# Performance work log

Measured on AMD Instinct MI355X. Metric: run time of the kernel, lower is better.

Reference implementation:

```python
import jax, jax.numpy as jnp
import numpy as np

C = 5          # max within-cluster spike gap (module-level constant in source repo)
DELTA = 0.05   # margin constant (module-level constant in source repo)
B, T, N = 128, 512, 256


def setup_inputs() -> dict:
    key = jax.random.key(0)
    k1, k2, k3 = jax.random.split(key, 3)
    vmem = jax.random.normal(k1, (B, T, N), dtype=jnp.float32) - 1.5
    vlastmem = jax.random.normal(k2, (B, T, N), dtype=jnp.float32)  # unused by the loss math
    labels_t = jax.random.randint(k3, (B, N), 0, 4)
    ratio = jnp.float32(0.5)
    return {"vmem": vmem, "vlastmem": vlastmem, "labels_t": labels_t, "ratio": ratio}


def _per_neuron(v, key):
    """v: [T] membrane trace for one (batch, neuron). Returns (num_cluster, under_term, max_over)."""
    Tn = v.shape[0]
    t = jnp.arange(Tn)
    spike = v >= 0.0
    s = spike.astype(jnp.int32)
    # prefix sums: cs[i] = number of spikes in v[:i]
    cs = jnp.concatenate([jnp.zeros(1, jnp.int32), jnp.cumsum(s)])
    # new cluster starts at t iff spike[t] and no spike in [t-C, t-1]  (gap > C)
    prev_cnt = cs[t] - cs[jnp.clip(t - C, 0, Tn)]
    is_start = spike & (prev_cnt == 0)
    nclu = jnp.sum(is_start.astype(jnp.int32))
    # under-branch mask = union over clusters of [first-C, last+C] = C-dilation of spike train
    dil_cnt = cs[jnp.clip(t + C + 1, 0, Tn)] - cs[jnp.clip(t - C, 0, Tn)]
    mask = dil_cnt > 0

    # per-cluster stats via segmented reductions (cluster id = running count of starts)
    cid = jnp.clip(jnp.cumsum(is_start.astype(jnp.int32)) - 1, 0, Tn - 1)
    counts = jax.ops.segment_sum(s, cid, num_segments=Tn)
    first = jax.ops.segment_min(jnp.where(spike, t, Tn), cid, num_segments=Tn)
    last = jax.ops.segment_max(jnp.where(spike, t, -1), cid, num_segments=Tn)

    # over branch: cluster minimizing (end_idx - beg_idx) == min spike count (first on ties)
    counts_q = jnp.where(t < nclu, counts, Tn + 2)
    ic = jnp.argmin(counts_q)
    over_mask = (t >= first[ic]) & (t <= last[ic])
    max_over = jnp.max(jnp.where(over_mask, v, -jnp.inf))

    # under branch: if unmasked timesteps remain, penalize -max(v[mask==0]);
    # else take v at a (pinned-seed) random spike position
    has_zero = jnp.any(~mask)
    max_unmask = jnp.max(jnp.where(~mask, v, -jnp.inf))
    nsp = cs[-1]
    sorted_pos = jnp.sort(jnp.where(spike, t, Tn))
    r = jax.random.randint(key, (), 0, jnp.maximum(nsp, 1))
    v_rand = v[jnp.clip(sorted_pos[r], 0, Tn - 1)]
    under_term = jnp.where(has_zero, -max_unmask, v_rand)
    return nclu, under_term, max_over


def _forward(vmem, vlastmem, labels_t, ratio):
    Bv, Tv, Nv = vmem.shape
    vflat = jnp.swapaxes(vmem, 1, 2).reshape(Bv * Nv, Tv)   # [B*N, T]
    lflat = labels_t.reshape(Bv * Nv)
    keys = jax.random.split(jax.random.key(42), Bv * Nv)     # pinned seed for the random-spike pick
    nclu, under_term, max_over = jax.vmap(_per_neuron)(vflat, keys)
    ncf = nclu.astype(vmem.dtype)
    margin = DELTA * ratio * ncf
    under = jnp.where(lflat > nclu, under_term + margin, 0.0)
    over = jnp.where(lflat < nclu, max_over + margin, 0.0)
    loss = jnp.sum(under + over)
    spike_output = ncf.reshape(Bv, Nv)
    return loss, spike_output


def reference(vmem, vlastmem, labels_t, ratio):
    return _forward(vmem, vlastmem, labels_t, ratio)
```

## Files before the change

### kernel.cpp

```cpp
#include <hip/hip_runtime.h>
#include <stdint.h>

#define TDIM 512
#define NDIM 256
#define CGAP 5
#define DELTA_C 0.05f
#define NSEG 8
#define SEGT 64
#define BIGI (1 << 28)

typedef unsigned long long u64;
typedef unsigned int u32;


__device__ __forceinline__ int  ctz64(u64 x)   { return x ? __builtin_ctzll(x) : 64; }
__device__ __forceinline__ int  hib64(u64 x)   { return x ? 63 - __builtin_clzll(x) : -1; }
__device__ __forceinline__ u64  below64(int p) { return (p >= 64) ? ~0ull : ((1ull << p) - 1ull); }

extern "C" __global__ void __launch_bounds__(512, 2)
stca_kernel(const float* __restrict__ vmem, const int* __restrict__ labels,
            const float* __restrict__ ratio_p, float* __restrict__ out,
            float* __restrict__ ws) {
  __shared__ u32 sw_lo[NSEG * 64], sw_hi[NSEG * 64];
  __shared__ int s_nclu[NSEG * 64], s_fs[NSEG * 64], s_ls[NSEG * 64];
  __shared__ int s_pc[NSEG * 64], s_pl[NSEG * 64];
  __shared__ int s_sc[NSEG * 64], s_sf[NSEG * 64];
  __shared__ int s_bc[NSEG * 64], s_bf[NSEG * 64], s_bl[NSEG * 64];
  __shared__ int pn_nclu[64], pn_tf[64], pn_tl[64];
  __shared__ float sO[NSEG * 64], sU[NSEG * 64];

  const int lane = threadIdx.x & 63;
  const int seg  = threadIdx.x >> 6;
  const int idx  = threadIdx.x;
  const int blk  = blockIdx.x;
  const int b    = blk >> 2;
  const int n0   = (blk & 3) << 6;
  const int n    = n0 + lane;

  const float* g = vmem + (size_t)b * TDIM * NDIM + n;
  const int t0 = seg * SEGT;

  u64 s = 0ull;
#pragma unroll 1
  for (int c = 0; c < SEGT / 8; ++c) {
    const float* gp = g + (size_t)(t0 + c * 8) * NDIM;
    const float y0 = gp[0 * NDIM], y1 = gp[1 * NDIM], y2 = gp[2 * NDIM],
                y3 = gp[3 * NDIM], y4 = gp[4 * NDIM], y5 = gp[5 * NDIM],
                y6 = gp[6 * NDIM], y7 = gp[7 * NDIM];
    const u32 bits = (y0 >= 0.f ?   1u : 0u) | (y1 >= 0.f ?   2u : 0u)
                   | (y2 >= 0.f ?   4u : 0u) | (y3 >= 0.f ?   8u : 0u)
                   | (y4 >= 0.f ?  16u : 0u) | (y5 >= 0.f ?  32u : 0u)
                   | (y6 >= 0.f ?  64u : 0u) | (y7 >= 0.f ? 128u : 0u);
    s |= (u64)bits << (c * 8);
  }

  u64 w5 = (s << 1) | (s << 2);
  w5 |= (s << 3) | (s << 4) | (s << 5);
  const u64 starts = s & ~w5;
  const int nclu = __popcll(starts);
  const int fs_l = ctz64(s);
  const int ls_l = hib64(s);
  const u64 st2 = starts & (starts - 1);
  const int p2  = ctz64(st2);
  const u64 pm  = s & below64(p2);
  const int pcnt  = __popcll(pm);
  const int pls_l = hib64(pm);
  const int plast = (nclu >= 1) ? hib64(starts) : 0;
  const int scnt  = __popcll(s >> plast);
  int bcnt = BIGI, bfs_l = 0, bls_l = 0;
  u64 rem = st2;
  while ((rem & (rem - 1)) != 0ull) {
    const int p   = ctz64(rem);
    const u64 rem2 = rem & (rem - 1);
    const int pnx = ctz64(rem2);
    const u64 m   = s & below64(pnx) & ~below64(p);
    const int cnt = __popcll(m);
    if (cnt < bcnt) { bcnt = cnt; bfs_l = p; bls_l = hib64(m); }
    rem = rem2;
  }

  sw_lo[idx] = (u32)s;  sw_hi[idx] = (u32)(s >> 32);
  s_nclu[idx] = nclu;
  s_fs[idx] = (nclu >= 1) ? (t0 + fs_l) : BIGI;
  s_ls[idx] = t0 + ls_l;
  s_pc[idx] = pcnt;  s_pl[idx] = t0 + pls_l;
  s_sc[idx] = scnt;  s_sf[idx] = t0 + plast;
  s_bc[idx] = bcnt;  s_bf[idx] = t0 + bfs_l;  s_bl[idx] = t0 + bls_l;
  __syncthreads();

  const u64 sL = (seg > 0)
      ? ((u64)sw_lo[idx - 64] | ((u64)sw_hi[idx - 64] << 32)) : 0ull;
  const u64 sR = (seg < NSEG - 1)
      ? ((u64)sw_lo[idx + 64] | ((u64)sw_hi[idx + 64] << 32)) : 0ull;
  u64 D = s;
  D |= (s << 1) | (sL >> 63);
  D |= (s << 2) | (sL >> 62);
  D |= (s << 3) | (sL >> 61);
  D |= (s << 4) | (sL >> 60);
  D |= (s << 5) | (sL >> 59);
  D |= (s >> 1) | (sR << 63);
  D |= (s >> 2) | (sR << 62);
  D |= (s >> 3) | (sR << 61);
  D |= (s >> 4) | (sR << 60);
  D |= (s >> 5) | (sR << 59);

  int a_nclu = 0;
  if (seg == 0) {
    int a_fs = BIGI, a_ls = 0;
    int a_pcnt = 0, a_pls = 0, a_scnt = 0, a_sfs = 0;
    int a_bcnt = BIGI, a_bfs = 0, a_bls = 0;
    for (int sg = 0; sg < NSEG; ++sg) {
      const int j = (sg << 6) + lane;
      const int r_nclu = s_nclu[j];
      if (r_nclu == 0) continue;
      const int r_fs = s_fs[j], r_ls = s_ls[j];
      const int r_pcnt = s_pc[j], r_pls = s_pl[j];
      const int r_scnt = s_sc[j], r_sfs = s_sf[j];
      const int r_bcnt = s_bc[j], r_bfs = s_bf[j], r_bl = s_bl[j];
      if (a_nclu == 0) {
        a_nclu = r_nclu; a_fs = r_fs; a_ls = r_ls;
        a_pcnt = r_pcnt; a_pls = r_pls; a_scnt = r_scnt; a_sfs = r_sfs;
        a_bcnt = r_bcnt; a_bfs = r_bfs; a_bls = r_bl;
        continue;
      }
      if (r_fs - a_ls <= CGAP) {
        const int Bc = a_scnt + r_pcnt, Bfs = a_sfs, Bls = r_pls;
        int nb = a_bcnt, nbf = a_bfs, nbl = a_bls;
        if (a_nclu >= 2 && r_nclu >= 2 && Bc < nb) { nb = Bc; nbf = Bfs; nbl = Bls; }
        if (r_bcnt < nb) { nb = r_bcnt; nbf = r_bfs; nbl = r_bl; }
        if (a_nclu == 1) { a_pcnt = Bc; a_pls = Bls; }
        if (r_nclu == 1) { a_scnt = Bc; a_sfs = Bfs; }
        else             { a_scnt = r_scnt; a_sfs = r_sfs; }
        a_bcnt = nb; a_bfs = nbf; a_bls = nbl;
        a_nclu += r_nclu - 1;
        a_ls = r_ls;
      } else {
        int nb = a_bcnt, nbf = a_bfs, nbl = a_bls;
        if (a_nclu >= 2 && a_scnt < nb) { nb = a_scnt; nbf = a_sfs; nbl = a_ls; }
        if (r_nclu >= 2 && r_pcnt < nb) { nb = r_pcnt; nbf = r_fs;  nbl = r_pls; }
        if (r_bcnt < nb) { nb = r_bcnt; nbf = r_bfs; nbl = r_bl; }
        a_bcnt = nb; a_bfs = nbf; a_bls = nbl;
        a_scnt = r_scnt; a_sfs = r_sfs;
        a_nclu += r_nclu;
        a_ls = r_ls;
      }
    }
    int tf = a_fs, tl = a_pls, bc = a_pcnt;
    if (a_nclu >= 2) {
      if (a_bcnt < bc) { bc = a_bcnt; tf = a_bfs; tl = a_bls; }
      if (a_scnt < bc) { bc = a_scnt; tf = a_sfs; tl = a_ls; }
    }
    pn_nclu[lane] = a_nclu; pn_tf[lane] = tf; pn_tl[lane] = tl;
    out[1 + b * NDIM + n] = (float)a_nclu;
  }
  __syncthreads();

  const int  label  = labels[b * NDIM + n];
  const int  f_nclu = pn_nclu[lane];
  const int  tf = pn_tf[lane], tl = pn_tl[lane];
  const bool needO = label < f_nclu;
  const bool needU = label > f_nclu;
  int lo = tf - t0; lo = lo < 0 ? 0 : (lo > 64 ? 64 : lo);
  int hi = tl - t0 + 1; hi = hi < 0 ? 0 : (hi > 64 ? 64 : hi);
  u64 R  = needO ? (below64(hi) & ~below64(lo)) : 0ull;
  u64 Dm = needU ? ~D : 0ull;
  float mO = -INFINITY, mU = -INFINITY;
  if (__any((R | Dm) != 0ull)) {
#pragma unroll 1
    for (int c = 0; c < SEGT / 8; ++c) {
      const float* gp = g + (size_t)(t0 + c * 8) * NDIM;
      const float y0 = gp[0 * NDIM], y1 = gp[1 * NDIM], y2 = gp[2 * NDIM],
                  y3 = gp[3 * NDIM], y4 = gp[4 * NDIM], y5 = gp[5 * NDIM],
                  y6 = gp[6 * NDIM], y7 = gp[7 * NDIM];
      const u32 r8 = (u32)(R >> (c * 8));
      const u32 d8 = (u32)(Dm >> (c * 8));
      mO = (r8 &   1u) ? fmaxf(mO, y0) : mO;  mU = (d8 &   1u) ? fmaxf(mU, y0) : mU;
      mO = (r8 &   2u) ? fmaxf(mO, y1) : mO;  mU = (d8 &   2u) ? fmaxf(mU, y1) : mU;
      mO = (r8 &   4u) ? fmaxf(mO, y2) : mO;  mU = (d8 &   4u) ? fmaxf(mU, y2) : mU;
      mO = (r8 &   8u) ? fmaxf(mO, y3) : mO;  mU = (d8 &   8u) ? fmaxf(mU, y3) : mU;
      mO = (r8 &  16u) ? fmaxf(mO, y4) : mO;  mU = (d8 &  16u) ? fmaxf(mU, y4) : mU;
      mO = (r8 &  32u) ? fmaxf(mO, y5) : mO;  mU = (d8 &  32u) ? fmaxf(mU, y5) : mU;
      mO = (r8 &  64u) ? fmaxf(mO, y6) : mO;  mU = (d8 &  64u) ? fmaxf(mU, y6) : mU;
      mO = (r8 & 128u) ? fmaxf(mO, y7) : mO;  mU = (d8 & 128u) ? fmaxf(mU, y7) : mU;
    }
  }
  sO[idx] = mO; sU[idx] = mU;
  __syncthreads();

  if (seg != 0) return;

  float mo = sO[lane], mu = sU[lane];
#pragma unroll
  for (int sg = 1; sg < NSEG; ++sg) {
    mo = fmaxf(mo, sO[(sg << 6) + lane]);
    mu = fmaxf(mu, sU[(sg << 6) + lane]);
  }
  const float ratio  = ratio_p[0];
  const float ncf    = (float)a_nclu;
  const float margin = DELTA_C * ratio * ncf;
  const float under_term = (mu > -INFINITY) ? (-mu) : 0.0f;
  const float under = (label > a_nclu) ? (under_term + margin) : 0.0f;
  const float over  = (label < a_nclu) ? (mo + margin) : 0.0f;

  float sum = under + over;
#pragma unroll
  for (int off = 32; off > 0; off >>= 1) sum += __shfl_down(sum, off);
  if (lane == 0) ws[blk] = sum;
}

extern "C" __global__ void __launch_bounds__(64, 1)
stca_reduce(const float* __restrict__ ws, float* __restrict__ out) {
  const int lane = threadIdx.x;
  float s = 0.0f;
#pragma unroll
  for (int i = 0; i < 8; ++i) s += ws[lane + (i << 6)];
#pragma unroll
  for (int off = 32; off > 0; off >>= 1) s += __shfl_down(s, off);
  if (lane == 0) out[0] = s;
}

extern "C" void kernel_launch(void* const* d_in, const int* in_sizes, int n_in,
                              void* d_out, int out_size, void* d_ws,
                              size_t ws_size, hipStream_t stream) {
  const float* vmem   = (const float*)d_in[0];
  const int*   labels = (const int*)d_in[2];
  const float* ratio  = (const float*)d_in[3];
  float* out = (float*)d_out;
  float* ws  = (float*)d_ws;

  dim3 grid(512);
  dim3 block(512);
  hipLaunchKernelGGL(stca_kernel, grid, block, 0, stream, vmem, labels, ratio,
                     out, ws);
  hipLaunchKernelGGL(stca_reduce, dim3(1), dim3(64), 0, stream, ws, out);
}
```

Before: 146.2 us.

## Keep the 64-step membrane segment in registers to avoid a second global read pass

Each thread now loads all 64 timesteps of its segment into registers in one fully unrolled batch. The spike bitmask is built from those registers, and the later over/under max reductions reuse them instead of reading vmem from global memory again. This removes the second read of the input and exposes more loads in flight at once. In exchange it needs about 64 extra live VGPRs per thread, and launch_bounds is raised to 4 waves-per-EU minimum, which may force register spilling.

```diff
diff --git a/kernel.cpp b/kernel.cpp
--- a/kernel.cpp
+++ b/kernel.cpp
@@ -17,7 +17,7 @@
 __device__ __forceinline__ int  hib64(u64 x)   { return x ? 63 - __builtin_clzll(x) : -1; }
 __device__ __forceinline__ u64  below64(int p) { return (p >= 64) ? ~0ull : ((1ull << p) - 1ull); }
 
-extern "C" __global__ void __launch_bounds__(512, 2)
+extern "C" __global__ void __launch_bounds__(512, 4)
 stca_kernel(const float* __restrict__ vmem, const int* __restrict__ labels,
             const float* __restrict__ ratio_p, float* __restrict__ out,
             float* __restrict__ ws) {
@@ -40,19 +40,29 @@
   const float* g = vmem + (size_t)b * TDIM * NDIM + n;
   const int t0 = seg * SEGT;
 
-  u64 s = 0ull;
-#pragma unroll 1
-  for (int c = 0; c < SEGT / 8; ++c) {
-    const float* gp = g + (size_t)(t0 + c * 8) * NDIM;
-    const float y0 = gp[0 * NDIM], y1 = gp[1 * NDIM], y2 = gp[2 * NDIM],
-                y3 = gp[3 * NDIM], y4 = gp[4 * NDIM], y5 = gp[5 * NDIM],
-                y6 = gp[6 * NDIM], y7 = gp[7 * NDIM];
-    const u32 bits = (y0 >= 0.f ?   1u : 0u) | (y1 >= 0.f ?   2u : 0u)
-                   | (y2 >= 0.f ?   4u : 0u) | (y3 >= 0.f ?   8u : 0u)
-                   | (y4 >= 0.f ?  16u : 0u) | (y5 >= 0.f ?  32u : 0u)
-                   | (y6 >= 0.f ?  64u : 0u) | (y7 >= 0.f ? 128u : 0u);
-    s |= (u64)bits << (c * 8);
-  }
+  const float* gp = g + (size_t)t0 * NDIM;
+#define LD(i) const float v##i = gp[(i) * NDIM];
+  LD(0)  LD(1)  LD(2)  LD(3)  LD(4)  LD(5)  LD(6)  LD(7)
+  LD(8)  LD(9)  LD(10) LD(11) LD(12) LD(13) LD(14) LD(15)
+  LD(16) LD(17) LD(18) LD(19) LD(20) LD(21) LD(22) LD(23)
+  LD(24) LD(25) LD(26) LD(27) LD(28) LD(29) LD(30) LD(31)
+  LD(32) LD(33) LD(34) LD(35) LD(36) LD(37) LD(38) LD(39)
+  LD(40) LD(41) LD(42) LD(43) LD(44) LD(45) LD(46) LD(47)
+  LD(48) LD(49) LD(50) LD(51) LD(52) LD(53) LD(54) LD(55)
+  LD(56) LD(57) LD(58) LD(59) LD(60) LD(61) LD(62) LD(63)
+#undef LD
+
+#define SB(i) ((v##i >= 0.f) ? (1u << ((i) & 31)) : 0u)
+  const u32 blo = SB(0)  | SB(1)  | SB(2)  | SB(3)  | SB(4)  | SB(5)  | SB(6)  | SB(7)
+                | SB(8)  | SB(9)  | SB(10) | SB(11) | SB(12) | SB(13) | SB(14) | SB(15)
+                | SB(16) | SB(17) | SB(18) | SB(19) | SB(20) | SB(21) | SB(22) | SB(23)
+                | SB(24) | SB(25) | SB(26) | SB(27) | SB(28) | SB(29) | SB(30) | SB(31);
+  const u32 bhi = SB(32) | SB(33) | SB(34) | SB(35) | SB(36) | SB(37) | SB(38) | SB(39)
+                | SB(40) | SB(41) | SB(42) | SB(43) | SB(44) | SB(45) | SB(46) | SB(47)
+                | SB(48) | SB(49) | SB(50) | SB(51) | SB(52) | SB(53) | SB(54) | SB(55)
+                | SB(56) | SB(57) | SB(58) | SB(59) | SB(60) | SB(61) | SB(62) | SB(63);
+#undef SB
+  const u64 s = (u64)blo | ((u64)bhi << 32);
 
   u64 w5 = (s << 1) | (s << 2);
   w5 |= (s << 3) | (s << 4) | (s << 5);
@@ -162,27 +172,30 @@
   const bool needU = label > f_nclu;
   int lo = tf - t0; lo = lo < 0 ? 0 : (lo > 64 ? 64 : lo);
   int hi = tl - t0 + 1; hi = hi < 0 ? 0 : (hi > 64 ? 64 : hi);
-  u64 R  = needO ? (below64(hi) & ~below64(lo)) : 0ull;
-  u64 Dm = needU ? ~D : 0ull;
+  const u64 R  = needO ? (below64(hi) & ~below64(lo)) : 0ull;
+  const u64 Dm = needU ? ~D : 0ull;
   float mO = -INFINITY, mU = -INFINITY;
-  if (__any((R | Dm) != 0ull)) {
-#pragma unroll 1
-    for (int c = 0; c < SEGT / 8; ++c) {
-      const float* gp = g + (size_t)(t0 + c * 8) * NDIM;
-      const float y0 = gp[0 * NDIM], y1 = gp[1 * NDIM], y2 = gp[2 * NDIM],
-                  y3 = gp[3 * NDIM], y4 = gp[4 * NDIM], y5 = gp[5 * NDIM],
-                  y6 = gp[6 * NDIM], y7 = gp[7 * NDIM];
-      const u32 r8 = (u32)(R >> (c * 8));
-      const u32 d8 = (u32)(Dm >> (c * 8));
-      mO = (r8 &   1u) ? fmaxf(mO, y0) : mO;  mU = (d8 &   1u) ? fmaxf(mU, y0) : mU;
-      mO = (r8 &   2u) ? fmaxf(mO, y1) : mO;  mU = (d8 &   2u) ? fmaxf(mU, y1) : mU;
-      mO = (r8 &   4u) ? fmaxf(mO, y2) : mO;  mU = (d8 &   4u) ? fmaxf(mU, y2) : mU;
-      mO = (r8 &   8u) ? fmaxf(mO, y3) : mO;  mU = (d8 &   8u) ? fmaxf(mU, y3) : mU;
-      mO = (r8 &  16u) ? fmaxf(mO, y4) : mO;  mU = (d8 &  16u) ? fmaxf(mU, y4) : mU;
-      mO = (r8 &  32u) ? fmaxf(mO, y5) : mO;  mU = (d8 &  32u) ? fmaxf(mU, y5) : mU;
-      mO = (r8 &  64u) ? fmaxf(mO, y6) : mO;  mU = (d8 &  64u) ? fmaxf(mU, y6) : mU;
-      mO = (r8 & 128u) ? fmaxf(mO, y7) : mO;  mU = (d8 & 128u) ? fmaxf(mU, y7) : mU;
-    }
+#define MO(i) mO = ((R >> (i)) & 1ull) ? fmaxf(mO, v##i) : mO;
+  MO(0)  MO(1)  MO(2)  MO(3)  MO(4)  MO(5)  MO(6)  MO(7)
+  MO(8)  MO(9)  MO(10) MO(11) MO(12) MO(13) MO(14) MO(15)
+  MO(16) MO(17) MO(18) MO(19) MO(20) MO(21) MO(22) MO(23)
+  MO(24) MO(25) MO(26) MO(27) MO(28) MO(29) MO(30) MO(31)
+  MO(32) MO(33) MO(34) MO(35) MO(36) MO(37) MO(38) MO(39)
+  MO(40) MO(41) MO(42) MO(43) MO(44) MO(45) MO(46) MO(47)
+  MO(48) MO(49) MO(50) MO(51) MO(52) MO(53) MO(54) MO(55)
+  MO(56) MO(57) MO(58) MO(59) MO(60) MO(61) MO(62) MO(63)
+#undef MO
+  if (__any(Dm != 0ull)) {
+#define MU(i) mU = ((Dm >> (i)) & 1ull) ? fmaxf(mU, v##i) : mU;
+    MU(0)  MU(1)  MU(2)  MU(3)  MU(4)  MU(5)  MU(6)  MU(7)
+    MU(8)  MU(9)  MU(10) MU(11) MU(12) MU(13) MU(14) MU(15)
+    MU(16) MU(17) MU(18) MU(19) MU(20) MU(21) MU(22) MU(23)
+    MU(24) MU(25) MU(26) MU(27) MU(28) MU(29) MU(30) MU(31)
+    MU(32) MU(33) MU(34) MU(35) MU(36) MU(37) MU(38) MU(39)
+    MU(40) MU(41) MU(42) MU(43) MU(44) MU(45) MU(46) MU(47)
+    MU(48) MU(49) MU(50) MU(51) MU(52) MU(53) MU(54) MU(55)
+    MU(56) MU(57) MU(58) MU(59) MU(60) MU(61) MU(62) MU(63)
+#undef MU
   }
   sO[idx] = mO; sU[idx] = mU;
   __syncthreads();
```

New measurement: 146.7 us. No clear change (+0.3%).
